# Kernel optimization log

Hardware: AMD Instinct MI355X
Metric: run time of the kernel (lower is better)

Reference implementation:

```python
import jax, jax.numpy as jnp
import numpy as np

BUCKETS = 256


def _gru_cell(x, h, W_ih, W_hh, b_ih, b_hh):
    # torch GRUCell math, gate order (r, z, n)
    gi = x @ W_ih.T + b_ih            # [B, 3H]
    gh = h @ W_hh.T + b_hh            # [B, 3H]
    i_r, i_z, i_n = jnp.split(gi, 3, axis=-1)
    h_r, h_z, h_n = jnp.split(gh, 3, axis=-1)
    r = jax.nn.sigmoid(i_r + h_r)
    z = jax.nn.sigmoid(i_z + h_z)
    n = jnp.tanh(i_n + r * h_n)
    return (1.0 - z) * n + z * h


def setup_inputs() -> dict:
    key = jax.random.key(0)
    ks = jax.random.split(key, 10)
    B, T, C, G, H, V = 16, 2000, 128, 512, 512, BUCKETS
    s = 0.1  # keep gates in a sane range
    return {
        "cond": jax.random.normal(ks[0], (B, T, C), jnp.float32),
        "h0": jnp.zeros((B, G), jnp.float32),
        "W_ih": jax.random.normal(ks[1], (3 * G, C), jnp.float32) * s,
        "W_hh": jax.random.normal(ks[2], (3 * G, G), jnp.float32) * s,
        "b_ih": jax.random.normal(ks[3], (3 * G,), jnp.float32) * s,
        "b_hh": jax.random.normal(ks[4], (3 * G,), jnp.float32) * s,
        "W_hid": jax.random.normal(ks[5], (H, G), jnp.float32) * s,
        "b_hid": jax.random.normal(ks[6], (H,), jnp.float32) * s,
        "W_out": jax.random.normal(ks[7], (V, H), jnp.float32) * s,
        "b_out": jax.random.normal(ks[8], (V,), jnp.float32) * s,
        "embedding": jax.random.normal(ks[9], (V, C), jnp.float32) * s,
    }


def reference(cond, h0, W_ih, W_hh, b_ih, b_hh, W_hid, b_hid, W_out, b_out, embedding):
    B, T, C = cond.shape
    keys = jax.random.split(jax.random.key(1), T)
    prev0 = jnp.full((B,), BUCKETS // 2, jnp.int32)  # mid-bucket = mu-law zero

    def step(carry, inp):
        h, prev = carry
        cond_t, k = inp
        x = cond_t + embedding[prev]                  # [B, C]
        h = _gru_cell(x, h, W_ih, W_hh, b_ih, b_hh)   # [B, G]
        hid = jax.nn.relu(h @ W_hid.T + b_hid)        # [B, H]
        logits = hid @ W_out.T + b_out                # [B, V]
        sample = jax.random.categorical(k, logits, axis=-1).astype(jnp.int32)
        return (h, sample), (logits, sample)

    (h_final, _), (logits, samples) = jax.lax.scan(
        step, (h0, prev0), (jnp.swapaxes(cond, 0, 1), keys))
    # logits: [T, B, V] -> [B, T, V]; samples: [T, B] -> [B, T]
    return jnp.swapaxes(logits, 0, 1), jnp.swapaxes(samples, 0, 1), h_final
```

## Files before the change

kernel.cpp:

```cpp
#include <hip/hip_runtime.h>
#include <stdint.h>
#include <math.h>

#define NBLK 128
#define NTHR 256
#define Bn 16
#define Tn 2000
#define Cn 128
#define Gn 512
#define Hn 512
#define Vn 256

#define WS_DBL_BASE 512
#define GRP_STRIDE  3072

#define OUT_SAMP ((size_t)Bn*Tn*Vn)
#define OUT_HF   (OUT_SAMP + (size_t)Bn*Tn)

typedef __attribute__((ext_vector_type(2))) double d2_t;

__device__ __forceinline__ unsigned rotl32(unsigned v, int n) {
  return (v << n) | (v >> (32 - n));
}

__device__ __forceinline__ void threefry2x32(unsigned k0, unsigned k1,
                                             unsigned c0, unsigned c1,
                                             unsigned& o0, unsigned& o1) {
  unsigned ks2 = k0 ^ k1 ^ 0x1BD11BDAu;
  unsigned x0 = c0 + k0;
  unsigned x1 = c1 + k1;
#define TF_R(r) { x0 += x1; x1 = rotl32(x1, r); x1 ^= x0; }
  TF_R(13) TF_R(15) TF_R(26) TF_R(6)
  x0 += k1;  x1 += ks2 + 1u;
  TF_R(17) TF_R(29) TF_R(16) TF_R(24)
  x0 += ks2; x1 += k0 + 2u;
  TF_R(13) TF_R(15) TF_R(26) TF_R(6)
  x0 += k0;  x1 += k1 + 3u;
  TF_R(17) TF_R(29) TF_R(16) TF_R(24)
  x0 += k1;  x1 += ks2 + 4u;
  TF_R(13) TF_R(15) TF_R(26) TF_R(6)
  x0 += ks2; x1 += k0 + 5u;
#undef TF_R
  o0 = x0; o1 = x1;
}

__device__ __forceinline__ double jax_gumbel(unsigned kt0, unsigned kt1,
                                             unsigned f) {
  unsigned r0, r1;
  threefry2x32(kt0, kt1, 0u, f, r0, r1);
  unsigned bits = r0 ^ r1;
  float uf = __uint_as_float((bits >> 9) | 0x3f800000u) - 1.0f;
  if (uf <= 0.f) uf = 1.17549435e-38f;
  return -log(-log((double)uf));
}

__device__ __forceinline__ void st_d(double* p, double v) {
  asm volatile("global_store_dwordx2 %0, %1, off sc0 sc1"
               :: "v"(p), "v"(v) : "memory");
}
__device__ __forceinline__ d2_t ld_d2(const double* p) {
  d2_t r;
  asm volatile("global_load_dwordx4 %0, %1, off sc0 sc1\n\t"
               "s_waitcnt vmcnt(0)" : "=v"(r) : "v"(p));
  return r;
}
__device__ __forceinline__ void ld8(const double* pl, int v, double* o) {
  const double* a0 = pl + v;
  const double* a1 = pl + 512 + v;
  const double* a2 = pl + 1024 + v;
  const double* a3 = pl + 1536 + v;
  double o0, o1, o2, o3, o4, o5, o6, o7;
  asm volatile(
    "global_load_dwordx2 %[r0], %[p0], off sc0 sc1\n\t"
    "global_load_dwordx2 %[r1], %[p0], off offset:2048 sc0 sc1\n\t"
    "global_load_dwordx2 %[r2], %[p1], off sc0 sc1\n\t"
    "global_load_dwordx2 %[r3], %[p1], off offset:2048 sc0 sc1\n\t"
    "global_load_dwordx2 %[r4], %[p2], off sc0 sc1\n\t"
    "global_load_dwordx2 %[r5], %[p2], off offset:2048 sc0 sc1\n\t"
    "global_load_dwordx2 %[r6], %[p3], off sc0 sc1\n\t"
    "global_load_dwordx2 %[r7], %[p3], off offset:2048 sc0 sc1\n\t"
    "s_waitcnt vmcnt(0)"
    : [r0]"=v"(o0), [r1]"=v"(o1), [r2]"=v"(o2), [r3]"=v"(o3),
      [r4]"=v"(o4), [r5]"=v"(o5), [r6]"=v"(o6), [r7]"=v"(o7)
    : [p0]"v"(a0), [p1]"v"(a1), [p2]"v"(a2), [p3]"v"(a3));
  o[0]=o0; o[1]=o1; o[2]=o2; o[3]=o3; o[4]=o4; o[5]=o5; o[6]=o6; o[7]=o7;
}
__device__ __forceinline__ unsigned ld_u(const unsigned* p) {
  unsigned r;
  asm volatile("global_load_dword %0, %1, off sc0 sc1\n\t"
               "s_waitcnt vmcnt(0)" : "=v"(r) : "v"(p) : "memory");
  return r;
}
__device__ __forceinline__ void st_u(unsigned* p, unsigned v) {
  asm volatile("global_store_dword %0, %1, off sc0 sc1"
               :: "v"(p), "v"(v) : "memory");
}

__device__ __forceinline__ void gar(unsigned* flags, int slot, unsigned target) {
  asm volatile("s_waitcnt vmcnt(0)" ::: "memory");
  __syncthreads();
  if (threadIdx.x == 0) st_u(&flags[slot], target);
}
__device__ __forceinline__ void gwt(unsigned* flags, unsigned target) {
  if (threadIdx.x < 8) {
    int guard = 0;
    while (ld_u(&flags[threadIdx.x]) < target) {
      if (++guard > 5000000) break;
    }
  }
  asm volatile("" ::: "memory");
  __syncthreads();
}

extern "C" __global__ __launch_bounds__(NTHR)
void wavernn_pipe(const float* __restrict__ cond, const float* __restrict__ h0,
                  const float* __restrict__ W_ih, const float* __restrict__ W_hh,
                  const float* __restrict__ b_ih, const float* __restrict__ b_hh,
                  const float* __restrict__ W_hid, const float* __restrict__ b_hid,
                  const float* __restrict__ W_out, const float* __restrict__ b_out,
                  const float* __restrict__ emb,
                  float* __restrict__ out, double* __restrict__ ws) {
  const int tid = threadIdx.x;
  const int blk = blockIdx.x;
  const int g = blk >> 3;
  const int j = blk & 7;
  const int lane = tid & 63, wv = tid >> 6;

  unsigned* flags = ((unsigned*)ws) + (size_t)g * 64;
  double* G   = ws + WS_DBL_BASE + (size_t)g * GRP_STRIDE;
  double* Hb0 = G;
  double* Hb1 = G + 512;
  double* PL  = G + 1024;

  __shared__ __attribute__((aligned(32))) double s_x[Cn];
  __shared__ __attribute__((aligned(32))) double s_h[Gn];
  __shared__ __attribute__((aligned(32))) double s_hid[64];
  __shared__ double s_hn[64], s_in[64], s_z[64];
  __shared__ double s_part[4][64];
  __shared__ double s_gum[256];
  __shared__ float  s_cond[Cn];
  __shared__ double s_pv[4];
  __shared__ int    s_pi[4];

  if (tid < 64) st_d(&Hb0[j * 64 + tid],
                     (double)h0[(size_t)g * Gn + j * 64 + tid]);
  if (tid < Cn) s_x[tid] = (double)cond[(size_t)g * Tn * Cn + tid]
                         + (double)emb[128 * Cn + tid];
  gar(flags, j, 1u); gwt(flags, 1u);
  ((d2_t*)s_h)[tid] = ld_d2(Hb0 + 2 * tid);
  __syncthreads();

  for (int t = 0; t < Tn; ++t) {
    double* hnxt = (t & 1) ? Hb0 : Hb1;

    double ha0 = 0., ha1 = 0., ha2 = 0., ha3 = 0.;
    if (wv <= 2) {
      const int row = wv * 512 + j * 64 + lane;
      const float4* wh = (const float4*)(W_hh + (size_t)row * Gn);
      const double4* h4 = (const double4*)s_h;
#pragma unroll 8
      for (int k = 0; k < Gn / 4; ++k) {
        float4 w = wh[k]; double4 hv = h4[k];
        ha0 = fma((double)w.x, hv.x, ha0); ha1 = fma((double)w.y, hv.y, ha1);
        ha2 = fma((double)w.z, hv.z, ha2); ha3 = fma((double)w.w, hv.w, ha3);
      }
      if (wv == 2)
        s_hn[lane] = ((ha0 + ha1) + (ha2 + ha3)) + (double)b_hh[row];
    } else {
      const int c0 = 2 * lane;
      s_cond[c0]     = cond[((size_t)g * Tn + t) * Cn + c0];
      s_cond[c0 + 1] = cond[((size_t)g * Tn + t) * Cn + c0 + 1];
      if (t > 0) {
        unsigned kt0, kt1;
        threefry2x32(0u, 1u, 0u, (unsigned)(t - 1), kt0, kt1);
#pragma unroll
        for (int i = 0; i < 4; ++i) {
          int v = 4 * lane + i;
          s_gum[v] = jax_gumbel(kt0, kt1, (unsigned)(g * Vn + v));
        }
      }
    }

    if (t > 0) {
      gwt(flags, (unsigned)(2 * t + 1));
      const int v = tid;
      double l[8];
      ld8(PL, v, l);
      double logit = ((((((((l[0] + l[1]) + l[2]) + l[3]) + l[4]) + l[5])
                       + l[6]) + l[7])) + (double)b_out[v];
      if (j == 0)
        out[(size_t)g * Tn * Vn + (size_t)(t - 1) * Vn + v] = (float)logit;
      double bv = logit + s_gum[v];
      int bi = v;
#pragma unroll
      for (int off = 1; off < 64; off <<= 1) {
        double ov = __shfl_xor(bv, off, 64);
        int oi = __shfl_xor(bi, off, 64);
        if (ov > bv || (ov == bv && oi < bi)) { bv = ov; bi = oi; }
      }
      if (lane == 0) { s_pv[wv] = bv; s_pi[wv] = bi; }
      __syncthreads();
      double fv = s_pv[0]; int fi = s_pi[0];
#pragma unroll
      for (int w = 1; w < 4; ++w) {
        double ov = s_pv[w]; int oi = s_pi[w];
        if (ov > fv || (ov == fv && oi < fi)) { fv = ov; fi = oi; }
      }
      const int samp = fi;
      if (tid == 0 && j == 0)
        out[OUT_SAMP + (size_t)g * Tn + (t - 1)] = (float)samp;
      if (tid < Cn)
        s_x[tid] = (double)s_cond[tid] + (double)emb[(size_t)samp * Cn + tid];
      __syncthreads();
    } else {
      __syncthreads();
    }

    double r_reg = 0.;
    if (wv <= 1) {
      const int row = wv * 512 + j * 64 + lane;
      const float4* wi = (const float4*)(W_ih + (size_t)row * Cn);
      const double4* x4 = (const double4*)s_x;
      double xa0 = 0., xa1 = 0., xa2 = 0., xa3 = 0.;
#pragma unroll 8
      for (int k = 0; k < Cn / 4; ++k) {
        float4 w = wi[k]; double4 xv = x4[k];
        xa0 = fma((double)w.x, xv.x, xa0); xa1 = fma((double)w.y, xv.y, xa1);
        xa2 = fma((double)w.z, xv.z, xa2); xa3 = fma((double)w.w, xv.w, xa3);
      }
      double gi = ((xa0 + xa1) + (xa2 + xa3)) + (double)b_ih[row];
      double gh = ((ha0 + ha1) + (ha2 + ha3)) + (double)b_hh[row];
      double pre = gi + gh;
      double sig = 1.0 / (1.0 + exp(-pre));
      if (wv == 0) r_reg = sig; else s_z[lane] = sig;
    } else if (wv == 3) {
      const int row = 1024 + j * 64 + lane;
      const float4* wi = (const float4*)(W_ih + (size_t)row * Cn);
      const double4* x4 = (const double4*)s_x;
      double a0 = 0., a1 = 0., a2 = 0., a3 = 0.;
#pragma unroll 8
      for (int k = 0; k < Cn / 4; ++k) {
        float4 w = wi[k]; double4 xv = x4[k];
        a0 = fma((double)w.x, xv.x, a0); a1 = fma((double)w.y, xv.y, a1);
        a2 = fma((double)w.z, xv.z, a2); a3 = fma((double)w.w, xv.w, a3);
      }
      s_in[lane] = ((a0 + a1) + (a2 + a3)) + (double)b_ih[row];
    }
    __syncthreads();

    if (wv == 0) {
      double z = s_z[lane];
      double n = tanh(s_in[lane] + r_reg * s_hn[lane]);
      double hv = (1.0 - z) * n + z * s_h[j * 64 + lane];
      st_d(&hnxt[j * 64 + lane], hv);
    }
    gar(flags, j, (unsigned)(2 * t + 2));
    gwt(flags, (unsigned)(2 * t + 2));
    ((d2_t*)s_h)[tid] = ld_d2(hnxt + 2 * tid);
    __syncthreads();
    if (t == Tn - 1 && j == 0) {
      out[OUT_HF + (size_t)g * Gn + tid] = (float)s_h[tid];
      out[OUT_HF + (size_t)g * Gn + tid + 256] = (float)s_h[tid + 256];
    }

    {
      const int row = j * 64 + lane;
      const float4* wr = (const float4*)(W_hid + (size_t)row * Gn + wv * 128);
      const double4* hh = (const double4*)(s_h + wv * 128);
      double a0 = 0., a1 = 0., a2 = 0., a3 = 0.;
#pragma unroll 8
      for (int k = 0; k < 32; ++k) {
        float4 w = wr[k]; double4 hv = hh[k];
        a0 = fma((double)w.x, hv.x, a0); a1 = fma((double)w.y, hv.y, a1);
        a2 = fma((double)w.z, hv.z, a2); a3 = fma((double)w.w, hv.w, a3);
      }
      s_part[wv][lane] = (a0 + a1) + (a2 + a3);
    }
    __syncthreads();
    if (tid < 64) {
      double acc = (s_part[0][tid] + s_part[1][tid])
                 + (s_part[2][tid] + s_part[3][tid])
                 + (double)b_hid[j * 64 + tid];
      s_hid[tid] = acc > 0.0 ? acc : 0.0;
    }
    __syncthreads();
    {
      const int v = tid;
      const float4* wr = (const float4*)(W_out + (size_t)v * Hn + j * 64);
      const double4* hh = (const double4*)s_hid;
      double a0 = 0., a1 = 0., a2 = 0., a3 = 0.;
#pragma unroll 8
      for (int k = 0; k < 16; ++k) {
        float4 w = wr[k]; double4 hv = hh[k];
        a0 = fma((double)w.x, hv.x, a0); a1 = fma((double)w.y, hv.y, a1);
        a2 = fma((double)w.z, hv.z, a2); a3 = fma((double)w.w, hv.w, a3);
      }
      st_d(&PL[j * 256 + v], (a0 + a1) + (a2 + a3));
    }
    gar(flags, j, (unsigned)(2 * t + 3));
  }

  gwt(flags, (unsigned)(2 * Tn + 1));
  {
    const int v = tid;
    double l[8];
    ld8(PL, v, l);
    double logit = ((((((((l[0] + l[1]) + l[2]) + l[3]) + l[4]) + l[5])
                     + l[6]) + l[7])) + (double)b_out[v];
    if (j == 0)
      out[(size_t)g * Tn * Vn + (size_t)(Tn - 1) * Vn + v] = (float)logit;
    unsigned kt0, kt1;
    threefry2x32(0u, 1u, 0u, (unsigned)(Tn - 1), kt0, kt1);
    double gum = jax_gumbel(kt0, kt1, (unsigned)(g * Vn + v));
    double bv = logit + gum;
    int bi = v;
#pragma unroll
    for (int off = 1; off < 64; off <<= 1) {
      double ov = __shfl_xor(bv, off, 64);
      int oi = __shfl_xor(bi, off, 64);
      if (ov > bv || (ov == bv && oi < bi)) { bv = ov; bi = oi; }
    }
    if (lane == 0) { s_pv[wv] = bv; s_pi[wv] = bi; }
    __syncthreads();
    double fv = s_pv[0]; int fi = s_pi[0];
#pragma unroll
    for (int w = 1; w < 4; ++w) {
      double ov = s_pv[w]; int oi = s_pi[w];
      if (ov > fv || (ov == fv && oi < fi)) { fv = ov; fi = oi; }
    }
    if (tid == 0 && j == 0)
      out[OUT_SAMP + (size_t)g * Tn + (Tn - 1)] = (float)fi;
  }
}

extern "C" void kernel_launch(void* const* d_in, const int* in_sizes, int n_in,
                              void* d_out, int out_size, void* d_ws, size_t ws_size,
                              hipStream_t stream) {
  const float* cond  = (const float*)d_in[0];
  const float* h0    = (const float*)d_in[1];
  const float* W_ih  = (const float*)d_in[2];
  const float* W_hh  = (const float*)d_in[3];
  const float* b_ih  = (const float*)d_in[4];
  const float* b_hh  = (const float*)d_in[5];
  const float* W_hid = (const float*)d_in[6];
  const float* b_hid = (const float*)d_in[7];
  const float* W_out = (const float*)d_in[8];
  const float* b_out = (const float*)d_in[9];
  const float* emb   = (const float*)d_in[10];

  hipMemsetAsync(d_ws, 0, 4096, stream);
  hipLaunchKernelGGL(wavernn_pipe, dim3(NBLK), dim3(NTHR), 0, stream,
                     cond, h0, W_ih, W_hh, b_ih, b_hh, W_hid, b_hid,
                     W_out, b_out, emb, (float*)d_out, (double*)d_ws);
}
```

Before: 48.82 ms.

## Split GEMV dot products across lanes with shuffle transpose-reduce

```diff
diff --git a/kernel.cpp b/kernel.cpp
--- a/kernel.cpp
+++ b/kernel.cpp
@@ -58,12 +58,6 @@
   asm volatile("global_store_dwordx2 %0, %1, off sc0 sc1"
                :: "v"(p), "v"(v) : "memory");
 }
-__device__ __forceinline__ d2_t ld_d2(const double* p) {
-  d2_t r;
-  asm volatile("global_load_dwordx4 %0, %1, off sc0 sc1\n\t"
-               "s_waitcnt vmcnt(0)" : "=v"(r) : "v"(p));
-  return r;
-}
 __device__ __forceinline__ void ld8(const double* pl, int v, double* o) {
   const double* a0 = pl + v;
   const double* a1 = pl + 512 + v;
@@ -80,15 +74,32 @@
     "global_load_dwordx2 %[r6], %[p3], off sc0 sc1\n\t"
     "global_load_dwordx2 %[r7], %[p3], off offset:2048 sc0 sc1\n\t"
     "s_waitcnt vmcnt(0)"
-    : [r0]"=v"(o0), [r1]"=v"(o1), [r2]"=v"(o2), [r3]"=v"(o3),
-      [r4]"=v"(o4), [r5]"=v"(o5), [r6]"=v"(o6), [r7]"=v"(o7)
+    : [r0]"=&v"(o0), [r1]"=&v"(o1), [r2]"=&v"(o2), [r3]"=&v"(o3),
+      [r4]"=&v"(o4), [r5]"=&v"(o5), [r6]"=&v"(o6), [r7]"=&v"(o7)
     : [p0]"v"(a0), [p1]"v"(a1), [p2]"v"(a2), [p3]"v"(a3));
   o[0]=o0; o[1]=o1; o[2]=o2; o[3]=o3; o[4]=o4; o[5]=o5; o[6]=o6; o[7]=o7;
+}
+__device__ __forceinline__ void ldh(const double* hb, int lane, int row,
+                                    double* hc, double& hold) {
+  const double* cp = hb + 8 * lane;
+  const double* rp = hb + row;
+  d2_t c0, c1, c2, c3; double hv;
+  asm volatile(
+    "global_load_dwordx4 %[a], %[p], off sc0 sc1\n\t"
+    "global_load_dwordx4 %[b], %[p], off offset:16 sc0 sc1\n\t"
+    "global_load_dwordx4 %[c], %[p], off offset:32 sc0 sc1\n\t"
+    "global_load_dwordx4 %[d], %[p], off offset:48 sc0 sc1\n\t"
+    "global_load_dwordx2 %[h], %[q], off sc0 sc1\n\t"
+    "s_waitcnt vmcnt(0)"
+    : [a]"=&v"(c0), [b]"=&v"(c1), [c]"=&v"(c2), [d]"=&v"(c3), [h]"=&v"(hv)
+    : [p]"v"(cp), [q]"v"(rp));
+  hc[0]=c0.x; hc[1]=c0.y; hc[2]=c1.x; hc[3]=c1.y;
+  hc[4]=c2.x; hc[5]=c2.y; hc[6]=c3.x; hc[7]=c3.y; hold = hv;
 }
 __device__ __forceinline__ unsigned ld_u(const unsigned* p) {
   unsigned r;
   asm volatile("global_load_dword %0, %1, off sc0 sc1\n\t"
-               "s_waitcnt vmcnt(0)" : "=v"(r) : "v"(p) : "memory");
+               "s_waitcnt vmcnt(0)" : "=&v"(r) : "v"(p) : "memory");
   return r;
 }
 __device__ __forceinline__ void st_u(unsigned* p, unsigned v) {
@@ -112,7 +123,34 @@
   __syncthreads();
 }
 
-extern "C" __global__ __launch_bounds__(NTHR)
+__device__ __forceinline__ double reduce8(const double* p, int lane) {
+  double q[4];
+#pragma unroll
+  for (int m = 0; m < 4; ++m) {
+    double a = p[2*m], b = p[2*m+1];
+    double t = (lane & 1) ? a : b;
+    double u = __shfl_xor(t, 1, 64);
+    q[m] = ((lane & 1) ? b : a) + u;
+  }
+  double r[2];
+#pragma unroll
+  for (int m = 0; m < 2; ++m) {
+    double a = q[2*m], b = q[2*m+1];
+    double t = (lane & 2) ? a : b;
+    double u = __shfl_xor(t, 2, 64);
+    r[m] = ((lane & 2) ? b : a) + u;
+  }
+  double a = r[0], b = r[1];
+  double t = (lane & 4) ? a : b;
+  double u = __shfl_xor(t, 4, 64);
+  double f = ((lane & 4) ? b : a) + u;
+  f += __shfl_xor(f, 8, 64);
+  f += __shfl_xor(f, 16, 64);
+  f += __shfl_xor(f, 32, 64);
+  return f;
+}
+
+extern "C" __global__ __launch_bounds__(NTHR, 1)
 void wavernn_pipe(const float* __restrict__ cond, const float* __restrict__ h0,
                   const float* __restrict__ W_ih, const float* __restrict__ W_hh,
                   const float* __restrict__ b_ih, const float* __restrict__ b_hh,
@@ -125,6 +163,7 @@
   const int g = blk >> 3;
   const int j = blk & 7;
   const int lane = tid & 63, wv = tid >> 6;
+  const int grp8 = lane >> 3;
 
   unsigned* flags = ((unsigned*)ws) + (size_t)g * 64;
   double* G   = ws + WS_DBL_BASE + (size_t)g * GRP_STRIDE;
@@ -133,39 +172,61 @@
   double* PL  = G + 1024;
 
   __shared__ __attribute__((aligned(32))) double s_x[Cn];
-  __shared__ __attribute__((aligned(32))) double s_h[Gn];
+  __shared__ double s_hg[3][64];
+  __shared__ double s_xg[3][64];
+  __shared__ double s_hidraw[64];
   __shared__ __attribute__((aligned(32))) double s_hid[64];
-  __shared__ double s_hn[64], s_in[64], s_z[64];
-  __shared__ double s_part[4][64];
   __shared__ double s_gum[256];
   __shared__ float  s_cond[Cn];
   __shared__ double s_pv[4];
   __shared__ int    s_pi[4];
+
+  const int rrow = j * 64 + lane;
+  double bih_r = 0., bih_z = 0., bih_n = 0.;
+  double bhh_r = 0., bhh_z = 0., bhh_n = 0., bhid = 0.;
+  if (wv == 0) {
+    bih_r = (double)b_ih[rrow]; bih_z = (double)b_ih[512 + rrow];
+    bih_n = (double)b_ih[1024 + rrow];
+    bhh_r = (double)b_hh[rrow]; bhh_z = (double)b_hh[512 + rrow];
+    bhh_n = (double)b_hh[1024 + rrow];
+    bhid  = (double)b_hid[rrow];
+  }
+  const double bout_reg = (double)b_out[tid];
+
+  double hc[8];
+  double hold = 0.;
 
   if (tid < 64) st_d(&Hb0[j * 64 + tid],
                      (double)h0[(size_t)g * Gn + j * 64 + tid]);
   if (tid < Cn) s_x[tid] = (double)cond[(size_t)g * Tn * Cn + tid]
                          + (double)emb[128 * Cn + tid];
   gar(flags, j, 1u); gwt(flags, 1u);
-  ((d2_t*)s_h)[tid] = ld_d2(Hb0 + 2 * tid);
-  __syncthreads();
+  ldh(Hb0, lane, rrow, hc, hold);
 
   for (int t = 0; t < Tn; ++t) {
     double* hnxt = (t & 1) ? Hb0 : Hb1;
 
-    double ha0 = 0., ha1 = 0., ha2 = 0., ha3 = 0.;
     if (wv <= 2) {
-      const int row = wv * 512 + j * 64 + lane;
-      const float4* wh = (const float4*)(W_hh + (size_t)row * Gn);
-      const double4* h4 = (const double4*)s_h;
-#pragma unroll 8
-      for (int k = 0; k < Gn / 4; ++k) {
-        float4 w = wh[k]; double4 hv = h4[k];
-        ha0 = fma((double)w.x, hv.x, ha0); ha1 = fma((double)w.y, hv.y, ha1);
-        ha2 = fma((double)w.z, hv.z, ha2); ha3 = fma((double)w.w, hv.w, ha3);
-      }
-      if (wv == 2)
-        s_hn[lane] = ((ha0 + ha1) + (ha2 + ha3)) + (double)b_hh[row];
+      const float* Wrow = W_hh + (size_t)(wv * 512 + j * 64) * Gn;
+      const float* lptr = Wrow + 8 * lane;
+#pragma unroll
+      for (int b = 0; b < 8; ++b) {
+        double p[8];
+#pragma unroll
+        for (int i = 0; i < 8; ++i) {
+          const float4 wlo = *(const float4*)(lptr + (size_t)i * Gn);
+          const float4 whi = *(const float4*)(lptr + (size_t)i * Gn + 4);
+          double s = 0.;
+          s = fma((double)wlo.x, hc[0], s); s = fma((double)wlo.y, hc[1], s);
+          s = fma((double)wlo.z, hc[2], s); s = fma((double)wlo.w, hc[3], s);
+          s = fma((double)whi.x, hc[4], s); s = fma((double)whi.y, hc[5], s);
+          s = fma((double)whi.z, hc[6], s); s = fma((double)whi.w, hc[7], s);
+          p[i] = s;
+        }
+        double f = reduce8(p, lane);
+        if (grp8 == b) s_hg[wv][lane] = f;
+        lptr += 8 * Gn;
+      }
     } else {
       const int c0 = 2 * lane;
       s_cond[c0]     = cond[((size_t)g * Tn + t) * Cn + c0];
@@ -187,7 +248,7 @@
       double l[8];
       ld8(PL, v, l);
       double logit = ((((((((l[0] + l[1]) + l[2]) + l[3]) + l[4]) + l[5])
-                       + l[6]) + l[7])) + (double)b_out[v];
+                       + l[6]) + l[7])) + bout_reg;
       if (j == 0)
         out[(size_t)g * Tn * Vn + (size_t)(t - 1) * Vn + v] = (float)logit;
       double bv = logit + s_gum[v];
@@ -216,86 +277,89 @@
       __syncthreads();
     }
 
-    double r_reg = 0.;
-    if (wv <= 1) {
-      const int row = wv * 512 + j * 64 + lane;
-      const float4* wi = (const float4*)(W_ih + (size_t)row * Cn);
-      const double4* x4 = (const double4*)s_x;
-      double xa0 = 0., xa1 = 0., xa2 = 0., xa3 = 0.;
-#pragma unroll 8
-      for (int k = 0; k < Cn / 4; ++k) {
-        float4 w = wi[k]; double4 xv = x4[k];
-        xa0 = fma((double)w.x, xv.x, xa0); xa1 = fma((double)w.y, xv.y, xa1);
-        xa2 = fma((double)w.z, xv.z, xa2); xa3 = fma((double)w.w, xv.w, xa3);
-      }
-      double gi = ((xa0 + xa1) + (xa2 + xa3)) + (double)b_ih[row];
-      double gh = ((ha0 + ha1) + (ha2 + ha3)) + (double)b_hh[row];
-      double pre = gi + gh;
-      double sig = 1.0 / (1.0 + exp(-pre));
-      if (wv == 0) r_reg = sig; else s_z[lane] = sig;
-    } else if (wv == 3) {
-      const int row = 1024 + j * 64 + lane;
-      const float4* wi = (const float4*)(W_ih + (size_t)row * Cn);
-      const double4* x4 = (const double4*)s_x;
-      double a0 = 0., a1 = 0., a2 = 0., a3 = 0.;
-#pragma unroll 8
-      for (int k = 0; k < Cn / 4; ++k) {
-        float4 w = wi[k]; double4 xv = x4[k];
-        a0 = fma((double)w.x, xv.x, a0); a1 = fma((double)w.y, xv.y, a1);
-        a2 = fma((double)w.z, xv.z, a2); a3 = fma((double)w.w, xv.w, a3);
-      }
-      s_in[lane] = ((a0 + a1) + (a2 + a3)) + (double)b_ih[row];
+    if (wv != 2) {
+      const int gi_ = (wv == 3) ? 2 : wv;
+      const double x0 = s_x[2 * lane], x1 = s_x[2 * lane + 1];
+      const float* Wrow = W_ih + (size_t)(gi_ * 512 + j * 64) * Cn;
+      const float* lptr = Wrow + 2 * lane;
+#pragma unroll
+      for (int b = 0; b < 8; ++b) {
+        double p[8];
+#pragma unroll
+        for (int i = 0; i < 8; ++i) {
+          const float2 w = *(const float2*)(lptr + (size_t)i * Cn);
+          p[i] = fma((double)w.x, x0, (double)w.y * x1);
+        }
+        double f = reduce8(p, lane);
+        if (grp8 == b) s_xg[gi_][lane] = f;
+        lptr += 8 * Cn;
+      }
     }
     __syncthreads();
 
     if (wv == 0) {
-      double z = s_z[lane];
-      double n = tanh(s_in[lane] + r_reg * s_hn[lane]);
-      double hv = (1.0 - z) * n + z * s_h[j * 64 + lane];
+      double hr = s_hg[0][lane] + bhh_r;
+      double hz = s_hg[1][lane] + bhh_z;
+      double hn = s_hg[2][lane] + bhh_n;
+      double xr = s_xg[0][lane] + bih_r;
+      double xz = s_xg[1][lane] + bih_z;
+      double xn = s_xg[2][lane] + bih_n;
+      double r = 1.0 / (1.0 + exp(-(xr + hr)));
+      double z = 1.0 / (1.0 + exp(-(xz + hz)));
+      double n = tanh(xn + r * hn);
+      double hv = (1.0 - z) * n + z * hold;
       st_d(&hnxt[j * 64 + lane], hv);
     }
     gar(flags, j, (unsigned)(2 * t + 2));
     gwt(flags, (unsigned)(2 * t + 2));
-    ((d2_t*)s_h)[tid] = ld_d2(hnxt + 2 * tid);
-    __syncthreads();
-    if (t == Tn - 1 && j == 0) {
-      out[OUT_HF + (size_t)g * Gn + tid] = (float)s_h[tid];
-      out[OUT_HF + (size_t)g * Gn + tid + 256] = (float)s_h[tid + 256];
+    ldh(hnxt, lane, rrow, hc, hold);
+    if (t == Tn - 1 && j == 0 && wv == 0) {
+#pragma unroll
+      for (int i = 0; i < 8; ++i)
+        out[OUT_HF + (size_t)g * Gn + 8 * lane + i] = (float)hc[i];
     }
 
     {
-      const int row = j * 64 + lane;
-      const float4* wr = (const float4*)(W_hid + (size_t)row * Gn + wv * 128);
-      const double4* hh = (const double4*)(s_h + wv * 128);
-      double a0 = 0., a1 = 0., a2 = 0., a3 = 0.;
-#pragma unroll 8
-      for (int k = 0; k < 32; ++k) {
-        float4 w = wr[k]; double4 hv = hh[k];
-        a0 = fma((double)w.x, hv.x, a0); a1 = fma((double)w.y, hv.y, a1);
-        a2 = fma((double)w.z, hv.z, a2); a3 = fma((double)w.w, hv.w, a3);
-      }
-      s_part[wv][lane] = (a0 + a1) + (a2 + a3);
+      const float* Wrow = W_hid + (size_t)(j * 64 + wv * 16) * Gn;
+      const float* lptr = Wrow + 8 * lane;
+#pragma unroll
+      for (int b = 0; b < 2; ++b) {
+        double p[8];
+#pragma unroll
+        for (int i = 0; i < 8; ++i) {
+          const float4 wlo = *(const float4*)(lptr + (size_t)i * Gn);
+          const float4 whi = *(const float4*)(lptr + (size_t)i * Gn + 4);
+          double s = 0.;
+          s = fma((double)wlo.x, hc[0], s); s = fma((double)wlo.y, hc[1], s);
+          s = fma((double)wlo.z, hc[2], s); s = fma((double)wlo.w, hc[3], s);
+          s = fma((double)whi.x, hc[4], s); s = fma((double)whi.y, hc[5], s);
+          s = fma((double)whi.z, hc[6], s); s = fma((double)whi.w, hc[7], s);
+          p[i] = s;
+        }
+        double f = reduce8(p, lane);
+        if (grp8 == 2 * wv + b) s_hidraw[lane] = f;
+        lptr += 8 * Gn;
+      }
     }
     __syncthreads();
     if (tid < 64) {
-      double acc = (s_part[0][tid] + s_part[1][tid])
-                 + (s_part[2][tid] + s_part[3][tid])
-                 + (double)b_hid[j * 64 + tid];
+      double acc = s_hidraw[tid] + bhid;
       s_hid[tid] = acc > 0.0 ? acc : 0.0;
     }
     __syncthreads();
     {
-      const int v = tid;
-      const float4* wr = (const float4*)(W_out + (size_t)v * Hn + j * 64);
-      const double4* hh = (const double4*)s_hid;
-      double a0 = 0., a1 = 0., a2 = 0., a3 = 0.;
-#pragma unroll 8
-      for (int k = 0; k < 16; ++k) {
-        float4 w = wr[k]; double4 hv = hh[k];
-        a0 = fma((double)w.x, hv.x, a0); a1 = fma((double)w.y, hv.y, a1);
-        a2 = fma((double)w.z, hv.z, a2); a3 = fma((double)w.w, hv.w, a3);
-      }
-      st_d(&PL[j * 256 + v], (a0 + a1) + (a2 + a3));
+      const double hidl = s_hid[lane];
+      const float* lptr = W_out + (size_t)(wv * 64) * Hn + j * 64 + lane;
+#pragma unroll
+      for (int b = 0; b < 8; ++b) {
+        double p[8];
+#pragma unroll
+        for (int i = 0; i < 8; ++i)
+          p[i] = (double)lptr[(size_t)i * Hn] * hidl;
+        double f = reduce8(p, lane);
+        if (grp8 == b) st_d(&PL[j * 256 + wv * 64 + lane], f);
+        lptr += (size_t)8 * Hn;
+      }
     }
     gar(flags, j, (unsigned)(2 * t + 3));
   }
@@ -306,7 +370,7 @@
     double l[8];
     ld8(PL, v, l);
     double logit = ((((((((l[0] + l[1]) + l[2]) + l[3]) + l[4]) + l[5])
-                     + l[6]) + l[7])) + (double)b_out[v];
+                     + l[6]) + l[7])) + bout_reg;
     if (j == 0)
       out[(size_t)g * Tn * Vn + (size_t)(Tn - 1) * Vn + v] = (float)logit;
     unsigned kt0, kt1;
```

Result: slower. 73.53 ms (+50.6%).
